# Performance work log

Measured on AMD Instinct MI355X. Metric: run time of the kernel, lower is better.

The kernel has to match this reference:

```python
import jax, jax.numpy as jnp
import numpy as np

SLOPE = 0.01   # torch LeakyReLU default negative_slope
TASK_TYPE = 2
N, E = 50000, 800000
IN, EMB, OUT, EF = 128, 128, 128, 64


def leaky(x):
    return jnp.where(x >= 0, x, SLOPE * x)


def setup_inputs() -> dict:
    key = jax.random.key(0)
    ks = jax.random.split(key, 12)
    nf = jax.random.normal(ks[0], (N, IN), jnp.float32)
    ef = jax.random.normal(ks[1], (E, EF), jnp.float32)
    src = jax.random.randint(ks[2], (E,), 0, N)
    dst = jax.random.randint(ks[3], (E,), 0, N)
    ntype = jax.random.randint(ks[4], (N,), 0, 4)
    # layer dims: (in, out) per GNNLayer
    dims = [(IN, EMB), (EMB, EMB), (EMB, OUT)]
    inp = {"nf": nf, "ef": ef, "src": src, "dst": dst, "ntype": ntype}
    for i, (di, do) in enumerate(dims):
        inp[f"W_edge_{i}"] = jax.random.normal(ks[5 + i], (2 * di + EF, do), jnp.float32) / np.sqrt(2 * di + EF)
        inp[f"W_node_{i}"] = jax.random.normal(ks[8 + i], (di + do, do), jnp.float32) / np.sqrt(di + do)
    return inp


def gnn_layer(nf, ef, We, Wn, src, dst, active, recv):
    # message: concat(src_nf, dst_nf, ef) -> Linear(no bias) -> LeakyReLU, only on edges from task nodes
    m_in = jnp.concatenate([nf[src], nf[dst], ef], axis=-1)   # [E, 2*di+EF]
    msg = leaky(m_in @ We) * active[:, None]                  # [E, do]
    # reduce: sum messages at destination nodes
    red = jax.ops.segment_sum(msg, dst, num_segments=nf.shape[0])  # [N, do]
    # apply: concat(nf, red_msg) -> Linear(no bias) -> LeakyReLU; only receiving nodes updated (others zero, DGL default)
    out = leaky(jnp.concatenate([nf, red], axis=-1) @ Wn) * recv[:, None]
    return out


def reference(nf, ef, W_edge_0, W_edge_1, W_edge_2, W_node_0, W_node_1, W_node_2, src, dst, ntype):
    active = (ntype[src] == TASK_TYPE).astype(nf.dtype)       # edges emitted by push(u=task_nodes)
    recv = (jax.ops.segment_sum(active, dst, num_segments=nf.shape[0]) > 0).astype(nf.dtype)
    Wes = [W_edge_0, W_edge_1, W_edge_2]
    Wns = [W_node_0, W_node_1, W_node_2]
    h = nf
    for We, Wn in zip(Wes, Wns):
        h = gnn_layer(h, ef, We, Wn, src, dst, active, recv)  # residual=False
    return h
```

## Files before the change

### kernel.cpp

```cpp
#include <hip/hip_runtime.h>

typedef unsigned short u16;
typedef short s16x8 __attribute__((ext_vector_type(8)));
typedef float f32x4 __attribute__((ext_vector_type(4)));

#define SLOPE 0.01f
#define EPB 64

__device__ __forceinline__ float leaky(float x) { return x >= 0.f ? x : SLOPE * x; }

__device__ __forceinline__ u16 f2b(float f) {
    union { float f; unsigned u; } v; v.f = f;
    unsigned r = v.u + 0x7FFFu + ((v.u >> 16) & 1u);
    return (u16)(r >> 16);
}
__device__ __forceinline__ float b2f(u16 b) {
    union { unsigned u; float f; } v; v.u = ((unsigned)b) << 16; return v.f;
}

__global__ __launch_bounds__(256) void k_init(
    const int* __restrict__ src, const int* __restrict__ dst,
    const int* __restrict__ ntype, int* __restrict__ deg,
    float* __restrict__ recvf, int* __restrict__ tflag, int E, int N)
{
    int i = blockIdx.x * 256 + threadIdx.x;
    if (i < E) {
        if (ntype[src[i]] == 2) {
            int d = dst[i];
            atomicAdd(&deg[d], 1);
            recvf[d] = 1.0f;
        }
    } else {
        int j = i - E;
        if (j < N) tflag[j] = (ntype[j] == 2) ? 1 : 0;
    }
}

__global__ __launch_bounds__(256) void k_scan1(
    const int* __restrict__ deg, const int* __restrict__ tflag,
    int* __restrict__ bsum, int* __restrict__ bsum2, int n)
{
    __shared__ int s[256];
    const int* v = blockIdx.y ? tflag : deg;
    int* out = blockIdx.y ? bsum2 : bsum;
    int i = blockIdx.x * 256 + threadIdx.x;
    s[threadIdx.x] = (i < n) ? v[i] : 0;
    __syncthreads();
    for (int o = 128; o > 0; o >>= 1) {
        if (threadIdx.x < o) s[threadIdx.x] += s[threadIdx.x + o];
        __syncthreads();
    }
    if (threadIdx.x == 0) out[blockIdx.x] = s[0];
}

__global__ __launch_bounds__(256) void k_scan2(
    int* __restrict__ bsum, int* __restrict__ bsum2, int nb,
    int* __restrict__ cntp, int* __restrict__ tcntp)
{
    __shared__ int s[256];
    int* arr = blockIdx.x ? bsum2 : bsum;
    int* tot = blockIdx.x ? tcntp : cntp;
    int v = (threadIdx.x < nb) ? arr[threadIdx.x] : 0;
    s[threadIdx.x] = v;
    __syncthreads();
    for (int o = 1; o < 256; o <<= 1) {
        int x = (threadIdx.x >= o) ? s[threadIdx.x - o] : 0;
        __syncthreads();
        s[threadIdx.x] += x;
        __syncthreads();
    }
    if (threadIdx.x < nb) arr[threadIdx.x] = s[threadIdx.x] - v;
    if (threadIdx.x == 255) *tot = s[255];
}

__global__ __launch_bounds__(256) void k_scan3(
    const int* __restrict__ deg, const int* __restrict__ tflag,
    const int* __restrict__ bsum, const int* __restrict__ bsum2,
    int* __restrict__ cursor, int* __restrict__ trank,
    int* __restrict__ tlist, int n)
{
    __shared__ int s[256];
    const int sel = blockIdx.y;
    const int* v = sel ? tflag : deg;
    const int* bexcl = sel ? bsum2 : bsum;
    int i = blockIdx.x * 256 + threadIdx.x;
    int x = (i < n) ? v[i] : 0;
    s[threadIdx.x] = x;
    __syncthreads();
    for (int o = 1; o < 256; o <<= 1) {
        int y = (threadIdx.x >= o) ? s[threadIdx.x - o] : 0;
        __syncthreads();
        s[threadIdx.x] += y;
        __syncthreads();
    }
    if (i < n) {
        int off = bexcl[blockIdx.x] + s[threadIdx.x] - x;
        if (sel) {
            trank[i] = off;
            if (x) tlist[off] = i;
        } else {
            cursor[i] = off;
        }
    }
}

__global__ __launch_bounds__(256) void k_scatter_pos(
    const int* __restrict__ src, const int* __restrict__ dst,
    const int* __restrict__ ntype, const int* __restrict__ trank,
    int* __restrict__ cursor, int* __restrict__ eS,
    int* __restrict__ sSg, int E)
{
    int e = blockIdx.x * 256 + threadIdx.x;
    if (e < E) {
        int s = src[e];
        if (ntype[s] == 2) {
            int d = dst[e];
            int p = atomicAdd(&cursor[d], 1);
            eS[p] = e; sSg[p] = trank[s];
        }
    }
}

__global__ __launch_bounds__(256) void k_efgather(
    const float* __restrict__ ef, const int* __restrict__ eS,
    const int* __restrict__ cntp, u16* __restrict__ efS)
{
    const int cnt = *cntp;
    const int b0 = blockIdx.x * 64;
    if (b0 >= cnt) return;
    const int t = threadIdx.x;
    #pragma unroll
    for (int pz = 0; pz < 4; ++pz) {
        int idx = t + pz * 256;
        int edge = idx >> 4, f4 = idx & 15;
        int p = b0 + edge;
        if (p < cnt) {
            float4 v = *(const float4*)(ef + (size_t)eS[p] * 64 + f4 * 4);
            ushort4 o;
            o.x = f2b(v.x); o.y = f2b(v.y); o.z = f2b(v.z); o.w = f2b(v.w);
            *(ushort4*)(efS + (size_t)p * 64 + f4 * 4) = o;
        }
    }
}

__global__ __launch_bounds__(256) void k_prep(
    const float* __restrict__ nf, u16* __restrict__ hb0, int n4,
    const float* __restrict__ We0, const float* __restrict__ We1,
    const float* __restrict__ We2, const float* __restrict__ Wn0,
    const float* __restrict__ Wn1, const float* __restrict__ Wn2,
    u16* __restrict__ WTe, u16* __restrict__ WTn, u16* __restrict__ WTef)
{
    int i = blockIdx.x * 256 + threadIdx.x;
    if (i < n4) {
        float4 v = ((const float4*)nf)[i];
        ushort4 o;
        o.x = f2b(v.x); o.y = f2b(v.y); o.z = f2b(v.z); o.w = f2b(v.w);
        ((ushort4*)hb0)[i] = o;
        return;
    }
    int j = i - n4;
    if (j >= 3 * 73728) return;
    int l = j / 73728;
    int idx = j - l * 73728;
    const float* We = (l == 0) ? We0 : (l == 1) ? We1 : We2;
    const float* Wn = (l == 0) ? Wn0 : (l == 1) ? Wn1 : Wn2;
    if (idx < 32768) {
        int sel = idx >> 14, jj = idx & 16383;
        int k = jj >> 7, n = jj & 127;
        WTe[(size_t)l * 32768 + sel * 16384 + n * 128 + k] = f2b(We[sel * 16384 + jj]);
    } else if (idx < 65536) {
        int jj = idx - 32768;
        int k = jj >> 7, n = jj & 127;
        WTn[(size_t)l * 32768 + n * 256 + k] = f2b(Wn[jj]);
    } else {
        int jj = idx - 65536;
        int k = jj >> 7, n = jj & 127;
        WTef[(size_t)l * 8192 + n * 64 + k] = f2b(We[32768 + jj]);
    }
}

__global__ __launch_bounds__(256) void k_gemm_T2(
    const u16* __restrict__ A, const u16* __restrict__ WTe_l,
    u16* __restrict__ Tsrc, u16* __restrict__ Tdst,
    const int* __restrict__ tlist, const int* __restrict__ tcntp, int Nfull)
{
    __shared__ u16 As[128][72];
    __shared__ u16 Bs[128][72];
    const int sel = blockIdx.y;
    const int M = sel ? Nfull : *tcntp;
    const int m0 = blockIdx.x * 128;
    if (m0 >= M) return;
    const u16* WT = WTe_l + sel * 16384;
    u16* T = sel ? Tdst : Tsrc;
    const int t = threadIdx.x;
    const int w = t >> 6, lane = t & 63, wm = w >> 1, wn = w & 1;
    f32x4 acc[4][4] = {};

    const int row = t >> 1, koff = (t & 1) * 32;
    const int gm_s = m0 + row;
    int arow = gm_s;
    if (!sel && gm_s < M) arow = tlist[gm_s];

    for (int kt = 0; kt < 128; kt += 64) {
        #pragma unroll
        for (int j = 0; j < 4; ++j) {
            int4 va = make_int4(0, 0, 0, 0);
            if (gm_s < M) va = *(const int4*)(A + (size_t)arow * 128 + kt + koff + j * 8);
            *(int4*)&As[row][koff + j * 8] = va;
            *(int4*)&Bs[row][koff + j * 8] =
                *(const int4*)(WT + (size_t)row * 128 + kt + koff + j * 8);
        }
        __syncthreads();
        #pragma unroll
        for (int kf = 0; kf < 2; ++kf) {
            s16x8 a[4], b[4];
            #pragma unroll
            for (int mi = 0; mi < 4; ++mi)
                a[mi] = *(const s16x8*)&As[wm * 64 + mi * 16 + (lane & 15)][kf * 32 + (lane >> 4) * 8];
            #pragma unroll
            for (int ni = 0; ni < 4; ++ni)
                b[ni] = *(const s16x8*)&Bs[wn * 64 + ni * 16 + (lane & 15)][kf * 32 + (lane >> 4) * 8];
            #pragma unroll
            for (int mi = 0; mi < 4; ++mi)
                #pragma unroll
                for (int ni = 0; ni < 4; ++ni)
                    acc[mi][ni] = __builtin_amdgcn_mfma_f32_16x16x32_bf16(
                        a[mi], b[ni], acc[mi][ni], 0, 0, 0);
        }
        __syncthreads();
    }
    const int lr = (lane >> 4) * 4, lc = lane & 15;
    #pragma unroll
    for (int mi = 0; mi < 4; ++mi) {
        #pragma unroll
        for (int r = 0; r < 4; ++r) {
            int gm = m0 + wm * 64 + mi * 16 + lr + r;
            if (gm < M) {
                #pragma unroll
                for (int ni = 0; ni < 4; ++ni)
                    T[(size_t)gm * 128 + wn * 64 + ni * 16 + lc] = f2b(acc[mi][ni][r]);
            }
        }
    }
}

__global__ __launch_bounds__(256) void k_msg(
    const u16* __restrict__ efS, const u16* __restrict__ WTef,
    const int* __restrict__ cntp, u16* __restrict__ msgS)
{
    __shared__ u16 Ms[64][136];
    const int cnt = *cntp;
    const int b0 = blockIdx.x * EPB;
    if (b0 >= cnt) return;
    const int t = threadIdx.x;
    const int w = t >> 6, lane = t & 63;
    const int lo = lane & 15, q = lane >> 4;
    const int ei = w * 16 + lo;
    const int p = b0 + ei;

    f32x4 acc[8] = {};
    #pragma unroll
    for (int kf = 0; kf < 2; ++kf) {
        s16x8 b = {};
        if (p < cnt) b = *(const s16x8*)(efS + (size_t)p * 64 + kf * 32 + q * 8);
        #pragma unroll
        for (int mi = 0; mi < 8; ++mi) {
            s16x8 a = *(const s16x8*)(WTef + (size_t)(mi * 16 + lo) * 64 + kf * 32 + q * 8);
            acc[mi] = __builtin_amdgcn_mfma_f32_16x16x32_bf16(a, b, acc[mi], 0, 0, 0);
        }
    }
    #pragma unroll
    for (int mi = 0; mi < 8; ++mi) {
        ushort4 o;
        o.x = f2b(acc[mi][0]); o.y = f2b(acc[mi][1]);
        o.z = f2b(acc[mi][2]); o.w = f2b(acc[mi][3]);
        *(ushort4*)&Ms[ei][mi * 16 + q * 4] = o;
    }
    __syncthreads();
    #pragma unroll
    for (int pz = 0; pz < 4; ++pz) {
        int idx = t + pz * 256;
        int row = idx >> 4, c8 = idx & 15;
        int pp = b0 + row;
        if (pp < cnt)
            *(int4*)(msgS + (size_t)pp * 128 + c8 * 8) = *(const int4*)&Ms[row][c8 * 8];
    }
}

__global__ __launch_bounds__(256) void k_reduce(
    const u16* __restrict__ msgS, const u16* __restrict__ Tsrc,
    const u16* __restrict__ Tdst, const int* __restrict__ sSg,
    const int* __restrict__ deg, const int* __restrict__ segEnd,
    u16* __restrict__ redb, int N)
{
    const int w = threadIdx.x >> 6, lane = threadIdx.x & 63;
    const int d = blockIdx.x * 4 + w;
    if (d >= N) return;
    const int dg = deg[d];
    if (dg == 0) return;
    const int end = segEnd[d], beg = end - dg;

    unsigned td = *(const unsigned*)(Tdst + (size_t)d * 128 + lane * 2);
    const float td0 = b2f((u16)(td & 0xffff)), td1 = b2f((u16)(td >> 16));
    float a0 = 0.f, a1 = 0.f;
    for (int i = beg; i < end; ++i) {
        int s = sSg[i];
        unsigned m  = *(const unsigned*)(msgS + (size_t)i * 128 + lane * 2);
        unsigned ts = *(const unsigned*)(Tsrc + (size_t)s * 128 + lane * 2);
        a0 += leaky(b2f((u16)(m & 0xffff)) + b2f((u16)(ts & 0xffff)) + td0);
        a1 += leaky(b2f((u16)(m >> 16))    + b2f((u16)(ts >> 16))    + td1);
    }
    unsigned out = (unsigned)f2b(a0) | ((unsigned)f2b(a1) << 16);
    *(unsigned*)(redb + (size_t)d * 128 + lane * 2) = out;
}

__global__ __launch_bounds__(256) void k_gemm_node(
    const u16* __restrict__ H, const u16* __restrict__ R,
    const u16* __restrict__ WT, const float* __restrict__ recvf,
    u16* __restrict__ O16, float* __restrict__ O32, int fin, int M)
{
    __shared__ u16 As[128][72];
    __shared__ u16 Bs[128][72];
    const int t = threadIdx.x;
    const int m0 = blockIdx.x * 128;
    const int w = t >> 6, lane = t & 63, wm = w >> 1, wn = w & 1;
    f32x4 acc[4][4] = {};

    const int row = t >> 1, koff = (t & 1) * 32;
    const int gm_s = m0 + row;

    for (int kt = 0; kt < 256; kt += 64) {
        const u16* Ap = (kt < 128) ? (H + kt) : (R + (kt - 128));
        #pragma unroll
        for (int j = 0; j < 4; ++j) {
            int4 va = make_int4(0, 0, 0, 0);
            if (gm_s < M) va = *(const int4*)(Ap + (size_t)gm_s * 128 + koff + j * 8);
            *(int4*)&As[row][koff + j * 8] = va;
            *(int4*)&Bs[row][koff + j * 8] =
                *(const int4*)(WT + (size_t)row * 256 + kt + koff + j * 8);
        }
        __syncthreads();
        #pragma unroll
        for (int kf = 0; kf < 2; ++kf) {
            s16x8 a[4], b[4];
            #pragma unroll
            for (int mi = 0; mi < 4; ++mi)
                a[mi] = *(const s16x8*)&As[wm * 64 + mi * 16 + (lane & 15)][kf * 32 + (lane >> 4) * 8];
            #pragma unroll
            for (int ni = 0; ni < 4; ++ni)
                b[ni] = *(const s16x8*)&Bs[wn * 64 + ni * 16 + (lane & 15)][kf * 32 + (lane >> 4) * 8];
            #pragma unroll
            for (int mi = 0; mi < 4; ++mi)
                #pragma unroll
                for (int ni = 0; ni < 4; ++ni)
                    acc[mi][ni] = __builtin_amdgcn_mfma_f32_16x16x32_bf16(
                        a[mi], b[ni], acc[mi][ni], 0, 0, 0);
        }
        __syncthreads();
    }
    const int lr = (lane >> 4) * 4, lc = lane & 15;
    #pragma unroll
    for (int mi = 0; mi < 4; ++mi) {
        #pragma unroll
        for (int r = 0; r < 4; ++r) {
            int gm = m0 + wm * 64 + mi * 16 + lr + r;
            if (gm < M) {
                float rv = recvf[gm];
                #pragma unroll
                for (int ni = 0; ni < 4; ++ni) {
                    float val = leaky(acc[mi][ni][r]) * rv;
                    size_t o = (size_t)gm * 128 + wn * 64 + ni * 16 + lc;
                    if (fin) O32[o] = val;
                    else     O16[o] = f2b(val);
                }
            }
        }
    }
}

extern "C" void kernel_launch(void* const* d_in, const int* in_sizes, int n_in,
                              void* d_out, int out_size, void* d_ws, size_t ws_size,
                              hipStream_t stream)
{
    const float* nf    = (const float*)d_in[0];
    const float* ef    = (const float*)d_in[1];
    const int*   src   = (const int*)d_in[2];
    const int*   dst   = (const int*)d_in[3];
    const int*   ntype = (const int*)d_in[4];
    const float* We[3] = {(const float*)d_in[5], (const float*)d_in[7], (const float*)d_in[9]};
    const float* Wn[3] = {(const float*)d_in[6], (const float*)d_in[8], (const float*)d_in[10]};

    const int N = in_sizes[0] / 128;
    const int E = in_sizes[1] / 64;

    u16* Tsrc = (u16*)d_ws;
    u16* Tdst = Tsrc + (size_t)N * 128;
    u16* hb0  = Tdst + (size_t)N * 128;
    u16* hb1  = hb0 + (size_t)N * 128;
    u16* redb = hb1 + (size_t)N * 128;
    u16* WTe  = redb + (size_t)N * 128;
    u16* WTn  = WTe + 3 * 32768;
    u16* WTef = WTn + 3 * 32768;
    u16* efS  = WTef + 3 * 8192;
    u16* msgS = efS + (size_t)E * 64;
    float* recvf = (float*)(msgS + (size_t)E * 128);
    int* deg    = (int*)(recvf + N);
    int* cursor = deg + N;
    int* tflag  = cursor + N;
    int* trank  = tflag + N;
    int* tlist  = trank + N;
    int* bsum   = tlist + N;
    int* bsum2  = bsum + 256;
    int* cntp   = bsum2 + 256;
    int* tcntp  = cntp + 4;
    int* eS     = tcntp + 4;
    int* sSg    = eS + E;

    const int nb  = (N + 255) / 256;
    const int gEb = (E + 255) / 256;
    const int n4  = N * 128 / 4;

    hipMemsetAsync(recvf, 0, (size_t)N * 2 * sizeof(float), stream);

    k_init<<<(E + N + 255) / 256, 256, 0, stream>>>(src, dst, ntype, deg, recvf, tflag, E, N);
    k_scan1<<<dim3(nb, 2), 256, 0, stream>>>(deg, tflag, bsum, bsum2, N);
    k_scan2<<<2, 256, 0, stream>>>(bsum, bsum2, nb, cntp, tcntp);
    k_scan3<<<dim3(nb, 2), 256, 0, stream>>>(deg, tflag, bsum, bsum2, cursor, trank, tlist, N);
    k_scatter_pos<<<gEb, 256, 0, stream>>>(src, dst, ntype, trank, cursor, eS, sSg, E);
    k_efgather<<<(E + 63) / 64, 256, 0, stream>>>(ef, eS, cntp, efS);
    k_prep<<<(n4 + 3 * 73728 + 255) / 256, 256, 0, stream>>>(
        nf, hb0, n4, We[0], We[1], We[2], Wn[0], Wn[1], Wn[2], WTe, WTn, WTef);

    dim3 gG((N + 127) / 128);
    dim3 gT((N + 127) / 128, 2);
    int  gE = (E + EPB - 1) / EPB;
    int  gR = (N + 3) / 4;

    const u16* hIn[3]  = {hb0, hb1, hb0};
    u16*       hOut[3] = {hb1, hb0, hb1};
    for (int l = 0; l < 3; ++l) {
        int fin = (l == 2);
        k_gemm_T2<<<gT, 256, 0, stream>>>(hIn[l], WTe + (size_t)l * 32768,
                                          Tsrc, Tdst, tlist, tcntp, N);
        k_msg<<<gE, 256, 0, stream>>>(efS, WTef + (size_t)l * 8192, cntp, msgS);
        k_reduce<<<gR, 256, 0, stream>>>(msgS, Tsrc, Tdst, sSg, deg, cursor, redb, N);
        k_gemm_node<<<gG, 256, 0, stream>>>(hIn[l], redb, WTn + (size_t)l * 32768,
                                            recvf, hOut[l], (float*)d_out, fin, N);
    }
}
```

Before: 342.7 us.

## Merge T2 GEMM with edge-message kernel and fuse reduction into node GEMM

Two changes. First, the source/destination projection GEMM and the edge-feature message GEMM are combined into one launch, with the block index choosing which job a block runs. Second, the per-destination segmented reduction now runs inside the node-update GEMM: each block reduces its 128 rows into shared memory and feeds them straight to MFMA as the second K half, so the redb buffer and its global round trip are gone. The cost is far fewer waves during the latency-bound gather phase (one block per 128 nodes, each wave walking 32 nodes in sequence) and more LDS per block.

Result: slower. 503.0 us (+46.8%).

```diff
diff --git a/kernel.cpp b/kernel.cpp
--- a/kernel.cpp
+++ b/kernel.cpp
@@ -179,47 +179,188 @@
     }
 }
 
-__global__ __launch_bounds__(256) void k_gemm_T2(
+__global__ __launch_bounds__(256) void k_T2msg(
     const u16* __restrict__ A, const u16* __restrict__ WTe_l,
     u16* __restrict__ Tsrc, u16* __restrict__ Tdst,
-    const int* __restrict__ tlist, const int* __restrict__ tcntp, int Nfull)
+    const int* __restrict__ tlist, const int* __restrict__ tcntp,
+    const u16* __restrict__ efS, const u16* __restrict__ WTef_l,
+    const int* __restrict__ cntp, u16* __restrict__ msgS,
+    int Nfull, int nT2)
+{
+    __shared__ u16 sh[2 * 128 * 72];
+    const int t = threadIdx.x;
+    const int bx = blockIdx.x;
+    const int w = t >> 6, lane = t & 63;
+    const int lo = lane & 15, q = lane >> 4;
+
+    if (bx < 2 * nT2) {
+        u16 (*As)[72] = (u16(*)[72])sh;
+        u16 (*Bs)[72] = (u16(*)[72])(sh + 128 * 72);
+        const int sel = (bx >= nT2) ? 1 : 0;
+        const int M = sel ? Nfull : *tcntp;
+        const int m0 = (bx - sel * nT2) * 128;
+        if (m0 >= M) return;
+        const u16* WT = WTe_l + sel * 16384;
+        u16* T = sel ? Tdst : Tsrc;
+        const int wm = w >> 1, wn = w & 1;
+        f32x4 acc[4][4] = {};
+
+        const int row = t >> 1, koff = (t & 1) * 32;
+        const int gm_s = m0 + row;
+        int arow = gm_s;
+        if (!sel && gm_s < M) arow = tlist[gm_s];
+
+        for (int kt = 0; kt < 128; kt += 64) {
+            #pragma unroll
+            for (int j = 0; j < 4; ++j) {
+                int4 va = make_int4(0, 0, 0, 0);
+                if (gm_s < M) va = *(const int4*)(A + (size_t)arow * 128 + kt + koff + j * 8);
+                *(int4*)&As[row][koff + j * 8] = va;
+                *(int4*)&Bs[row][koff + j * 8] =
+                    *(const int4*)(WT + (size_t)row * 128 + kt + koff + j * 8);
+            }
+            __syncthreads();
+            #pragma unroll
+            for (int kf = 0; kf < 2; ++kf) {
+                s16x8 a[4], b[4];
+                #pragma unroll
+                for (int mi = 0; mi < 4; ++mi)
+                    a[mi] = *(const s16x8*)&As[wm * 64 + mi * 16 + lo][kf * 32 + q * 8];
+                #pragma unroll
+                for (int ni = 0; ni < 4; ++ni)
+                    b[ni] = *(const s16x8*)&Bs[wn * 64 + ni * 16 + lo][kf * 32 + q * 8];
+                #pragma unroll
+                for (int mi = 0; mi < 4; ++mi)
+                    #pragma unroll
+                    for (int ni = 0; ni < 4; ++ni)
+                        acc[mi][ni] = __builtin_amdgcn_mfma_f32_16x16x32_bf16(
+                            a[mi], b[ni], acc[mi][ni], 0, 0, 0);
+            }
+            __syncthreads();
+        }
+        const int lr = q * 4, lc = lo;
+        #pragma unroll
+        for (int mi = 0; mi < 4; ++mi) {
+            #pragma unroll
+            for (int r = 0; r < 4; ++r) {
+                int gm = m0 + wm * 64 + mi * 16 + lr + r;
+                if (gm < M) {
+                    #pragma unroll
+                    for (int ni = 0; ni < 4; ++ni)
+                        T[(size_t)gm * 128 + wn * 64 + ni * 16 + lc] = f2b(acc[mi][ni][r]);
+                }
+            }
+        }
+    } else {
+        u16 (*Ms)[136] = (u16(*)[136])sh;
+        const int cnt = *cntp;
+        const int b0 = (bx - 2 * nT2) * EPB;
+        if (b0 >= cnt) return;
+        const int ei = w * 16 + lo;
+        const int p = b0 + ei;
+
+        f32x4 acc[8] = {};
+        #pragma unroll
+        for (int kf = 0; kf < 2; ++kf) {
+            s16x8 b = {};
+            if (p < cnt) b = *(const s16x8*)(efS + (size_t)p * 64 + kf * 32 + q * 8);
+            #pragma unroll
+            for (int mi = 0; mi < 8; ++mi) {
+                s16x8 a = *(const s16x8*)(WTef_l + (size_t)(mi * 16 + lo) * 64 + kf * 32 + q * 8);
+                acc[mi] = __builtin_amdgcn_mfma_f32_16x16x32_bf16(a, b, acc[mi], 0, 0, 0);
+            }
+        }
+        #pragma unroll
+        for (int mi = 0; mi < 8; ++mi) {
+            ushort4 o;
+            o.x = f2b(acc[mi][0]); o.y = f2b(acc[mi][1]);
+            o.z = f2b(acc[mi][2]); o.w = f2b(acc[mi][3]);
+            *(ushort4*)&Ms[ei][mi * 16 + q * 4] = o;
+        }
+        __syncthreads();
+        #pragma unroll
+        for (int pz = 0; pz < 4; ++pz) {
+            int idx = t + pz * 256;
+            int rrow = idx >> 4, c8 = idx & 15;
+            int pp = b0 + rrow;
+            if (pp < cnt)
+                *(int4*)(msgS + (size_t)pp * 128 + c8 * 8) = *(const int4*)&Ms[rrow][c8 * 8];
+        }
+    }
+}
+
+__global__ __launch_bounds__(256) void k_node_fused(
+    const u16* __restrict__ H, const u16* __restrict__ msgS,
+    const u16* __restrict__ Tsrc, const u16* __restrict__ Tdst,
+    const int* __restrict__ sSg, const int* __restrict__ deg,
+    const int* __restrict__ segEnd, const u16* __restrict__ WT,
+    const float* __restrict__ recvf, u16* __restrict__ O16,
+    float* __restrict__ O32, int fin, int M)
 {
     __shared__ u16 As[128][72];
     __shared__ u16 Bs[128][72];
-    const int sel = blockIdx.y;
-    const int M = sel ? Nfull : *tcntp;
+    __shared__ u16 Rs[128][136];
+    const int t = threadIdx.x;
     const int m0 = blockIdx.x * 128;
-    if (m0 >= M) return;
-    const u16* WT = WTe_l + sel * 16384;
-    u16* T = sel ? Tdst : Tsrc;
-    const int t = threadIdx.x;
-    const int w = t >> 6, lane = t & 63, wm = w >> 1, wn = w & 1;
+    const int w = t >> 6, lane = t & 63;
+    const int lo = lane & 15, q = lane >> 4;
+
+    for (int k = 0; k < 32; ++k) {
+        int rrow = w * 32 + k;
+        int d = m0 + rrow;
+        if (d >= M) break;
+        unsigned outw = 0;
+        int dg = deg[d];
+        if (dg > 0) {
+            int end = segEnd[d], beg = end - dg;
+            unsigned td = *(const unsigned*)(Tdst + (size_t)d * 128 + lane * 2);
+            float td0 = b2f((u16)(td & 0xffff)), td1 = b2f((u16)(td >> 16));
+            float a0 = 0.f, a1 = 0.f;
+            for (int i = beg; i < end; ++i) {
+                int s = sSg[i];
+                unsigned m  = *(const unsigned*)(msgS + (size_t)i * 128 + lane * 2);
+                unsigned ts = *(const unsigned*)(Tsrc + (size_t)s * 128 + lane * 2);
+                a0 += leaky(b2f((u16)(m & 0xffff)) + b2f((u16)(ts & 0xffff)) + td0);
+                a1 += leaky(b2f((u16)(m >> 16))    + b2f((u16)(ts >> 16))    + td1);
+            }
+            outw = (unsigned)f2b(a0) | ((unsigned)f2b(a1) << 16);
+        }
+        *(unsigned*)&Rs[rrow][lane * 2] = outw;
+    }
+    __syncthreads();
+
+    const int wm = w >> 1, wn = w & 1;
     f32x4 acc[4][4] = {};
-
     const int row = t >> 1, koff = (t & 1) * 32;
     const int gm_s = m0 + row;
-    int arow = gm_s;
-    if (!sel && gm_s < M) arow = tlist[gm_s];
-
-    for (int kt = 0; kt < 128; kt += 64) {
-        #pragma unroll
-        for (int j = 0; j < 4; ++j) {
-            int4 va = make_int4(0, 0, 0, 0);
-            if (gm_s < M) va = *(const int4*)(A + (size_t)arow * 128 + kt + koff + j * 8);
-            *(int4*)&As[row][koff + j * 8] = va;
+
+    for (int kt = 0; kt < 256; kt += 64) {
+        if (kt < 128) {
+            #pragma unroll
+            for (int j = 0; j < 4; ++j) {
+                int4 va = make_int4(0, 0, 0, 0);
+                if (gm_s < M) va = *(const int4*)(H + (size_t)gm_s * 128 + kt + koff + j * 8);
+                *(int4*)&As[row][koff + j * 8] = va;
+            }
+        }
+        #pragma unroll
+        for (int j = 0; j < 4; ++j)
             *(int4*)&Bs[row][koff + j * 8] =
-                *(const int4*)(WT + (size_t)row * 128 + kt + koff + j * 8);
-        }
+                *(const int4*)(WT + (size_t)row * 256 + kt + koff + j * 8);
         __syncthreads();
         #pragma unroll
         for (int kf = 0; kf < 2; ++kf) {
             s16x8 a[4], b[4];
             #pragma unroll
-            for (int mi = 0; mi < 4; ++mi)
-                a[mi] = *(const s16x8*)&As[wm * 64 + mi * 16 + (lane & 15)][kf * 32 + (lane >> 4) * 8];
+            for (int mi = 0; mi < 4; ++mi) {
+                if (kt < 128)
+                    a[mi] = *(const s16x8*)&As[wm * 64 + mi * 16 + lo][kf * 32 + q * 8];
+                else
+                    a[mi] = *(const s16x8*)&Rs[wm * 64 + mi * 16 + lo][(kt - 128) + kf * 32 + q * 8];
+            }
             #pragma unroll
             for (int ni = 0; ni < 4; ++ni)
-                b[ni] = *(const s16x8*)&Bs[wn * 64 + ni * 16 + (lane & 15)][kf * 32 + (lane >> 4) * 8];
+                b[ni] = *(const s16x8*)&Bs[wn * 64 + ni * 16 + lo][kf * 32 + q * 8];
             #pragma unroll
             for (int mi = 0; mi < 4; ++mi)
                 #pragma unroll
@@ -229,136 +370,7 @@
         }
         __syncthreads();
     }
-    const int lr = (lane >> 4) * 4, lc = lane & 15;
-    #pragma unroll
-    for (int mi = 0; mi < 4; ++mi) {
-        #pragma unroll
-        for (int r = 0; r < 4; ++r) {
-            int gm = m0 + wm * 64 + mi * 16 + lr + r;
-            if (gm < M) {
-                #pragma unroll
-                for (int ni = 0; ni < 4; ++ni)
-                    T[(size_t)gm * 128 + wn * 64 + ni * 16 + lc] = f2b(acc[mi][ni][r]);
-            }
-        }
-    }
-}
-
-__global__ __launch_bounds__(256) void k_msg(
-    const u16* __restrict__ efS, const u16* __restrict__ WTef,
-    const int* __restrict__ cntp, u16* __restrict__ msgS)
-{
-    __shared__ u16 Ms[64][136];
-    const int cnt = *cntp;
-    const int b0 = blockIdx.x * EPB;
-    if (b0 >= cnt) return;
-    const int t = threadIdx.x;
-    const int w = t >> 6, lane = t & 63;
-    const int lo = lane & 15, q = lane >> 4;
-    const int ei = w * 16 + lo;
-    const int p = b0 + ei;
-
-    f32x4 acc[8] = {};
-    #pragma unroll
-    for (int kf = 0; kf < 2; ++kf) {
-        s16x8 b = {};
-        if (p < cnt) b = *(const s16x8*)(efS + (size_t)p * 64 + kf * 32 + q * 8);
-        #pragma unroll
-        for (int mi = 0; mi < 8; ++mi) {
-            s16x8 a = *(const s16x8*)(WTef + (size_t)(mi * 16 + lo) * 64 + kf * 32 + q * 8);
-            acc[mi] = __builtin_amdgcn_mfma_f32_16x16x32_bf16(a, b, acc[mi], 0, 0, 0);
-        }
-    }
-    #pragma unroll
-    for (int mi = 0; mi < 8; ++mi) {
-        ushort4 o;
-        o.x = f2b(acc[mi][0]); o.y = f2b(acc[mi][1]);
-        o.z = f2b(acc[mi][2]); o.w = f2b(acc[mi][3]);
-        *(ushort4*)&Ms[ei][mi * 16 + q * 4] = o;
-    }
-    __syncthreads();
-    #pragma unroll
-    for (int pz = 0; pz < 4; ++pz) {
-        int idx = t + pz * 256;
-        int row = idx >> 4, c8 = idx & 15;
-        int pp = b0 + row;
-        if (pp < cnt)
-            *(int4*)(msgS + (size_t)pp * 128 + c8 * 8) = *(const int4*)&Ms[row][c8 * 8];
-    }
-}
-
-__global__ __launch_bounds__(256) void k_reduce(
-    const u16* __restrict__ msgS, const u16* __restrict__ Tsrc,
-    const u16* __restrict__ Tdst, const int* __restrict__ sSg,
-    const int* __restrict__ deg, const int* __restrict__ segEnd,
-    u16* __restrict__ redb, int N)
-{
-    const int w = threadIdx.x >> 6, lane = threadIdx.x & 63;
-    const int d = blockIdx.x * 4 + w;
-    if (d >= N) return;
-    const int dg = deg[d];
-    if (dg == 0) return;
-    const int end = segEnd[d], beg = end - dg;
-
-    unsigned td = *(const unsigned*)(Tdst + (size_t)d * 128 + lane * 2);
-    const float td0 = b2f((u16)(td & 0xffff)), td1 = b2f((u16)(td >> 16));
-    float a0 = 0.f, a1 = 0.f;
-    for (int i = beg; i < end; ++i) {
-        int s = sSg[i];
-        unsigned m  = *(const unsigned*)(msgS + (size_t)i * 128 + lane * 2);
-        unsigned ts = *(const unsigned*)(Tsrc + (size_t)s * 128 + lane * 2);
-        a0 += leaky(b2f((u16)(m & 0xffff)) + b2f((u16)(ts & 0xffff)) + td0);
-        a1 += leaky(b2f((u16)(m >> 16))    + b2f((u16)(ts >> 16))    + td1);
-    }
-    unsigned out = (unsigned)f2b(a0) | ((unsigned)f2b(a1) << 16);
-    *(unsigned*)(redb + (size_t)d * 128 + lane * 2) = out;
-}
-
-__global__ __launch_bounds__(256) void k_gemm_node(
-    const u16* __restrict__ H, const u16* __restrict__ R,
-    const u16* __restrict__ WT, const float* __restrict__ recvf,
-    u16* __restrict__ O16, float* __restrict__ O32, int fin, int M)
-{
-    __shared__ u16 As[128][72];
-    __shared__ u16 Bs[128][72];
-    const int t = threadIdx.x;
-    const int m0 = blockIdx.x * 128;
-    const int w = t >> 6, lane = t & 63, wm = w >> 1, wn = w & 1;
-    f32x4 acc[4][4] = {};
-
-    const int row = t >> 1, koff = (t & 1) * 32;
-    const int gm_s = m0 + row;
-
-    for (int kt = 0; kt < 256; kt += 64) {
-        const u16* Ap = (kt < 128) ? (H + kt) : (R + (kt - 128));
-        #pragma unroll
-        for (int j = 0; j < 4; ++j) {
-            int4 va = make_int4(0, 0, 0, 0);
-            if (gm_s < M) va = *(const int4*)(Ap + (size_t)gm_s * 128 + koff + j * 8);
-            *(int4*)&As[row][koff + j * 8] = va;
-            *(int4*)&Bs[row][koff + j * 8] =
-                *(const int4*)(WT + (size_t)row * 256 + kt + koff + j * 8);
-        }
-        __syncthreads();
-        #pragma unroll
-        for (int kf = 0; kf < 2; ++kf) {
-            s16x8 a[4], b[4];
-            #pragma unroll
-            for (int mi = 0; mi < 4; ++mi)
-                a[mi] = *(const s16x8*)&As[wm * 64 + mi * 16 + (lane & 15)][kf * 32 + (lane >> 4) * 8];
-            #pragma unroll
-            for (int ni = 0; ni < 4; ++ni)
-                b[ni] = *(const s16x8*)&Bs[wn * 64 + ni * 16 + (lane & 15)][kf * 32 + (lane >> 4) * 8];
-            #pragma unroll
-            for (int mi = 0; mi < 4; ++mi)
-                #pragma unroll
-                for (int ni = 0; ni < 4; ++ni)
-                    acc[mi][ni] = __builtin_amdgcn_mfma_f32_16x16x32_bf16(
-                        a[mi], b[ni], acc[mi][ni], 0, 0, 0);
-        }
-        __syncthreads();
-    }
-    const int lr = (lane >> 4) * 4, lc = lane & 15;
+    const int lr = q * 4, lc = lo;
     #pragma unroll
     for (int mi = 0; mi < 4; ++mi) {
         #pragma unroll
@@ -397,8 +409,7 @@
     u16* Tdst = Tsrc + (size_t)N * 128;
     u16* hb0  = Tdst + (size_t)N * 128;
     u16* hb1  = hb0 + (size_t)N * 128;
-    u16* redb = hb1 + (size_t)N * 128;
-    u16* WTe  = redb + (size_t)N * 128;
+    u16* WTe  = hb1 + (size_t)N * 128;
     u16* WTn  = WTe + 3 * 32768;
     u16* WTef = WTn + 3 * 32768;
     u16* efS  = WTef + 3 * 8192;
@@ -419,6 +430,8 @@
     const int nb  = (N + 255) / 256;
     const int gEb = (E + 255) / 256;
     const int n4  = N * 128 / 4;
+    const int nT2 = (N + 127) / 128;
+    const int gM  = (E + EPB - 1) / EPB;
 
     hipMemsetAsync(recvf, 0, (size_t)N * 2 * sizeof(float), stream);
 
@@ -431,20 +444,15 @@
     k_prep<<<(n4 + 3 * 73728 + 255) / 256, 256, 0, stream>>>(
         nf, hb0, n4, We[0], We[1], We[2], Wn[0], Wn[1], Wn[2], WTe, WTn, WTef);
 
-    dim3 gG((N + 127) / 128);
-    dim3 gT((N + 127) / 128, 2);
-    int  gE = (E + EPB - 1) / EPB;
-    int  gR = (N + 3) / 4;
-
     const u16* hIn[3]  = {hb0, hb1, hb0};
     u16*       hOut[3] = {hb1, hb0, hb1};
     for (int l = 0; l < 3; ++l) {
         int fin = (l == 2);
-        k_gemm_T2<<<gT, 256, 0, stream>>>(hIn[l], WTe + (size_t)l * 32768,
-                                          Tsrc, Tdst, tlist, tcntp, N);
-        k_msg<<<gE, 256, 0, stream>>>(efS, WTef + (size_t)l * 8192, cntp, msgS);
-        k_reduce<<<gR, 256, 0, stream>>>(msgS, Tsrc, Tdst, sSg, deg, cursor, redb, N);
-        k_gemm_node<<<gG, 256, 0, stream>>>(hIn[l], redb, WTn + (size_t)l * 32768,
-                                            recvf, hOut[l], (float*)d_out, fin, N);
-    }
-}
+        k_T2msg<<<2 * nT2 + gM, 256, 0, stream>>>(
+            hIn[l], WTe + (size_t)l * 32768, Tsrc, Tdst, tlist, tcntp,
+            efS, WTef + (size_t)l * 8192, cntp, msgS, N, nT2);
+        k_node_fused<<<nT2, 256, 0, stream>>>(
+            hIn[l], msgS, Tsrc, Tdst, sSg, deg, cursor,
+            WTn + (size_t)l * 32768, recvf, hOut[l], (float*)d_out, fin, N);
+    }
+}
```
